# Kernel optimization log

Measured on AMD Instinct MI355X. Metric: run time of the kernel, lower is better.

Reference implementation:

```python
import jax, jax.numpy as jnp
import numpy as np

N_NODES = 50000   # gates in the circuit batch
N_HOPS = 100000   # number of k-hop cones
MAX_PI = 8        # max PIs per hop (padded, masked via stats == -1)
D = 128           # token_emb / hidden
D_FF = 4 * D      # cls_head hidden width (512)
TT = 64           # max_tt_len -> logits width
LN_EPS = 1e-5


def setup_inputs() -> dict:
    key = jax.random.key(0)
    ks = jax.random.split(key, 8)
    hf = jax.random.normal(ks[0], (N_NODES, D), jnp.float32)
    all_hop_pi = jax.random.randint(ks[1], (N_HOPS, MAX_PI), 0, N_NODES)
    # stats in {-1, 0, 1}; -1 marks an invalid (padded) PI slot
    all_hop_pi_stats = jax.random.randint(ks[2], (N_HOPS, MAX_PI), 0, 3) - 1
    all_hop_po = jax.random.randint(ks[3], (N_HOPS,), 0, N_NODES)
    w_q = jax.random.normal(ks[4], (D,), jnp.float32) / np.sqrt(D)
    W1 = jax.random.normal(ks[5], (D, D_FF), jnp.float32) / np.sqrt(D)
    b1 = jnp.zeros((D_FF,), jnp.float32)
    gamma = jnp.ones((D_FF,), jnp.float32)
    beta = jnp.zeros((D_FF,), jnp.float32)
    W2 = jax.random.normal(ks[6], (D_FF, TT), jnp.float32) / np.sqrt(D_FF)
    b2 = jnp.zeros((TT,), jnp.float32)
    return {
        'hf': hf, 'w_q': w_q, 'W1': W1, 'b1': b1, 'gamma': gamma,
        'beta': beta, 'W2': W2, 'b2': b2,
        'all_hop_pi': all_hop_pi, 'all_hop_pi_stats': all_hop_pi_stats,
        'all_hop_po': all_hop_po,
    }


def reference(hf, w_q, W1, b1, gamma, beta, W2, b2,
              all_hop_pi, all_hop_pi_stats, all_hop_po):
    # Per-hop gather: valid PI embeddings + PO embedding -> [H, P+1, D]
    pi_tok = hf[all_hop_pi]                       # [H, P, D]
    po_tok = hf[all_hop_po][:, None, :]           # [H, 1, D]
    tokens = jnp.concatenate([pi_tok, po_tok], axis=1)
    valid = jnp.concatenate(
        [all_hop_pi_stats != -1,
         jnp.ones((all_hop_po.shape[0], 1), bool)], axis=1)  # [H, P+1]
    # tf_Pooling: masked single-query attention pooling over the ragged set
    scores = jnp.einsum('hpd,d->hp', tokens, w_q) / jnp.sqrt(jnp.float32(D))
    scores = jnp.where(valid, scores, jnp.float32(-1e30))
    attn = jax.nn.softmax(scores, axis=-1)
    hop_hf = jnp.einsum('hp,hpd->hd', attn, tokens)  # [H, D]
    # cls_head: Linear(D, 4D) -> ReLU -> LayerNorm(4D) -> Linear(4D, TT)
    h = jax.nn.relu(hop_hf @ W1 + b1)
    mu = jnp.mean(h, axis=-1, keepdims=True)
    var = jnp.var(h, axis=-1, keepdims=True)
    h = (h - mu) * jax.lax.rsqrt(var + LN_EPS) * gamma + beta
    logits = h @ W2 + b2                           # [H, TT]
    return logits
```

## Files before the change

### kernel.cpp

```cpp
#include <hip/hip_runtime.h>
#include <hip/hip_bf16.h>
#include <math.h>

#define DIM 128
#define DFF 512
#define TTW 64
#define NPI 8
#define NTOK 9
#define POOL_HOPS 8
#define HEAD_HOPS 32

typedef __attribute__((ext_vector_type(8))) short short8;
typedef __attribute__((ext_vector_type(4))) float float4v;

__device__ __forceinline__ unsigned short f32_bf16(float f) {
    union { float f; unsigned u; } v; v.f = f;
    unsigned r = v.u + 0x7FFFu + ((v.u >> 16) & 1u);
    return (unsigned short)(r >> 16);
}
__device__ __forceinline__ float bf16lo_f32(unsigned u) {
    union { unsigned u; float f; } v; v.u = u << 16;
    return v.f;
}
__device__ __forceinline__ float bf16hi_f32(unsigned u) {
    union { unsigned u; float f; } v; v.u = u & 0xffff0000u;
    return v.f;
}
__device__ __forceinline__ unsigned pk_bf16(float a, float b) {
    __hip_bfloat162 h = __float22bfloat162_rn(float2{a, b});
    union { __hip_bfloat162 h; unsigned u; } cv; cv.h = h;
    return cv.u;
}

__global__ __launch_bounds__(256)
void prep_k(const float* __restrict__ hf, const float* __restrict__ W1,
            const float* __restrict__ W2, const int* __restrict__ pi,
            const int* __restrict__ stats,
            unsigned short* __restrict__ hf2, unsigned short* __restrict__ w1t,
            unsigned short* __restrict__ w2t, int* __restrict__ cpack,
            int n_hf, int B_HF, int n_pk)
{
    __shared__ float tile[32][33];
    const int b = blockIdx.x, t = threadIdx.x;
    if (b < B_HF) {
        int i = (b * 256 + t) * 4;
        if (i < n_hf) {
            float4v v = *(const float4v*)(hf + i);
            uint2 o;
            o.x = pk_bf16(v[0], v[1]);
            o.y = pk_bf16(v[2], v[3]);
            *(uint2*)(hf2 + i) = o;
        }
    } else if (b < B_HF + 64) {
        const int tb = b - B_HF;
        const int r0 = (tb & 3) * 32, c0 = (tb >> 2) * 32;
        const int ty = t >> 3, tx = t & 7;
        *(float4v*)&tile[ty][tx * 4] = *(const float4v*)(W1 + (r0 + ty) * DFF + c0 + tx * 4);
        __syncthreads();
        uint2 o;
        o.x = pk_bf16(tile[tx * 4 + 0][ty], tile[tx * 4 + 1][ty]);
        o.y = pk_bf16(tile[tx * 4 + 2][ty], tile[tx * 4 + 3][ty]);
        *(uint2*)(w1t + (c0 + ty) * DIM + r0 + tx * 4) = o;
    } else if (b < B_HF + 96) {
        const int tb = b - B_HF - 64;
        const int r0 = (tb & 15) * 32, c0 = (tb >> 4) * 32;
        const int ty = t >> 3, tx = t & 7;
        *(float4v*)&tile[ty][tx * 4] = *(const float4v*)(W2 + (r0 + ty) * TTW + c0 + tx * 4);
        __syncthreads();
        uint2 o;
        o.x = pk_bf16(tile[tx * 4 + 0][ty], tile[tx * 4 + 1][ty]);
        o.y = pk_bf16(tile[tx * 4 + 2][ty], tile[tx * 4 + 3][ty]);
        *(uint2*)(w2t + (c0 + ty) * DFF + r0 + tx * 4) = o;
    } else {
        const int pb = b - (B_HF + 96);
        int i = (pb * 256 + t) * 4;
        if (i < n_pk) {
            int4 p = *(const int4*)(pi + i);
            int4 s = *(const int4*)(stats + i);
            int4 o;
            o.x = p.x | (s.x == -1 ? (int)0x80000000 : 0);
            o.y = p.y | (s.y == -1 ? (int)0x80000000 : 0);
            o.z = p.z | (s.z == -1 ? (int)0x80000000 : 0);
            o.w = p.w | (s.w == -1 ? (int)0x80000000 : 0);
            *(int4*)(cpack + i) = o;
        }
    }
}

__global__ __launch_bounds__(256, 6)
void pool_k(const unsigned short* __restrict__ hf2,
            const float* __restrict__ w_q,
            const int* __restrict__ cpack,
            const int* __restrict__ po,
            unsigned short* __restrict__ pooled,
            int H)
{
    const int t = threadIdx.x;
    const int g = t >> 5, l = t & 31;
    const int hop = blockIdx.x * POOL_HOPS + g;
    if (hop >= H) return;

    const float4v wq4 = *(const float4v*)(w_q + l * 4);

    int idx[NTOK]; bool val[NTOK];
    {
        int4 c0 = *(const int4*)(cpack + hop * NPI);
        int4 c1 = *(const int4*)(cpack + hop * NPI + 4);
        idx[0]=c0.x & 0x7fffffff; val[0]=c0.x >= 0;
        idx[1]=c0.y & 0x7fffffff; val[1]=c0.y >= 0;
        idx[2]=c0.z & 0x7fffffff; val[2]=c0.z >= 0;
        idx[3]=c0.w & 0x7fffffff; val[3]=c0.w >= 0;
        idx[4]=c1.x & 0x7fffffff; val[4]=c1.x >= 0;
        idx[5]=c1.y & 0x7fffffff; val[5]=c1.y >= 0;
        idx[6]=c1.z & 0x7fffffff; val[6]=c1.z >= 0;
        idx[7]=c1.w & 0x7fffffff; val[7]=c1.w >= 0;
        idx[8]=po[hop]; val[8]=true;
    }
    uint2 tu[NTOK];
    #pragma unroll
    for (int p = 0; p < NTOK; ++p)
        tu[p] = *(const uint2*)(hf2 + (size_t)idx[p] * DIM + l * 4);

    float tok[NTOK][4];
    #pragma unroll
    for (int p = 0; p < NTOK; ++p) {
        tok[p][0] = bf16lo_f32(tu[p].x);
        tok[p][1] = bf16hi_f32(tu[p].x);
        tok[p][2] = bf16lo_f32(tu[p].y);
        tok[p][3] = bf16hi_f32(tu[p].y);
    }
    float sc[NTOK];
    #pragma unroll
    for (int p = 0; p < NTOK; ++p)
        sc[p] = tok[p][0]*wq4[0] + tok[p][1]*wq4[1]
              + tok[p][2]*wq4[2] + tok[p][3]*wq4[3];
    #pragma unroll
    for (int m = 1; m < 32; m <<= 1) {
        #pragma unroll
        for (int p = 0; p < NTOK; ++p) sc[p] += __shfl_xor(sc[p], m);
    }
    const float isd = 0.08838834764831845f;
    float mx = -1e30f;
    #pragma unroll
    for (int p = 0; p < NTOK; ++p) {
        sc[p] = val[p] ? sc[p] * isd : -1e30f;
        mx = fmaxf(mx, sc[p]);
    }
    float se = 0.f;
    #pragma unroll
    for (int p = 0; p < NTOK; ++p) { sc[p] = __expf(sc[p] - mx); se += sc[p]; }
    const float inv = 1.f / se;
    float a0=0.f, a1=0.f, a2=0.f, a3=0.f;
    #pragma unroll
    for (int p = 0; p < NTOK; ++p) {
        float a = sc[p] * inv;
        a0 += a * tok[p][0]; a1 += a * tok[p][1];
        a2 += a * tok[p][2]; a3 += a * tok[p][3];
    }
    uint2 o;
    o.x = pk_bf16(a0, a1);
    o.y = pk_bf16(a2, a3);
    *(uint2*)(pooled + (size_t)hop * DIM + l * 4) = o;
}

__global__ __launch_bounds__(256, 3)
void head_k(const unsigned short* __restrict__ pooled,
            const unsigned short* __restrict__ w1t,
            const float* __restrict__ b1,
            const float* __restrict__ gamma,
            const float* __restrict__ beta,
            const unsigned short* __restrict__ w2t,
            const float* __restrict__ b2,
            float* __restrict__ out,
            int H)
{
    __shared__ unsigned short Hsm[HEAD_HOPS][DFF + 8];
    __shared__ float part[2][16][4][2];

    const int t    = threadIdx.x;
    const int lane = t & 63;
    const int w    = t >> 6;
    const int row  = lane & 15;
    const int quad = lane >> 4;
    const int hop0 = blockIdx.x * HEAD_HOPS;

    float4v acc[8][2];
    #pragma unroll
    for (int mt = 0; mt < 8; ++mt) {
        acc[mt][0] = (float4v){0.f, 0.f, 0.f, 0.f};
        acc[mt][1] = (float4v){0.f, 0.f, 0.f, 0.f};
    }
    {
        short8 bfr[2][4];
        #pragma unroll
        for (int ks = 0; ks < 4; ++ks) {
            const int k0 = ks * 32 + quad * 8;
            #pragma unroll
            for (int ht = 0; ht < 2; ++ht) {
                int hp = hop0 + ht * 16 + row;
                if (hp >= H) hp = H - 1;
                bfr[ht][ks] = *(const short8*)(pooled + (size_t)hp * DIM + k0);
            }
        }
        #pragma unroll
        for (int mt = 0; mt < 8; ++mt) {
            const unsigned short* wrow = w1t + (size_t)(w * 128 + mt * 16 + row) * DIM;
            #pragma unroll
            for (int ks = 0; ks < 4; ++ks) {
                short8 afr = *(const short8*)(wrow + ks * 32 + quad * 8);
                acc[mt][0] = __builtin_amdgcn_mfma_f32_16x16x32_bf16(afr, bfr[0][ks], acc[mt][0], 0, 0, 0);
                acc[mt][1] = __builtin_amdgcn_mfma_f32_16x16x32_bf16(afr, bfr[1][ks], acc[mt][1], 0, 0, 0);
            }
        }
    }
    float sum0 = 0.f, ssq0 = 0.f, sum1 = 0.f, ssq1 = 0.f;
    #pragma unroll
    for (int mt = 0; mt < 8; ++mt) {
        const int nb = w * 128 + mt * 16 + quad * 4;
        const float4v bias = *(const float4v*)(b1 + nb);
        #pragma unroll
        for (int r = 0; r < 4; ++r) {
            float v0 = fmaxf(acc[mt][0][r] + bias[r], 0.f);
            float v1 = fmaxf(acc[mt][1][r] + bias[r], 0.f);
            acc[mt][0][r] = v0;  sum0 += v0;  ssq0 += v0 * v0;
            acc[mt][1][r] = v1;  sum1 += v1;  ssq1 += v1 * v1;
        }
    }
    #pragma unroll
    for (int m = 16; m <= 32; m <<= 1) {
        sum0 += __shfl_xor(sum0, m);  ssq0 += __shfl_xor(ssq0, m);
        sum1 += __shfl_xor(sum1, m);  ssq1 += __shfl_xor(ssq1, m);
    }
    if (lane < 16) {
        part[0][row][w][0] = sum0;  part[0][row][w][1] = ssq0;
        part[1][row][w][0] = sum1;  part[1][row][w][1] = ssq1;
    }
    __syncthreads();
    float mu[2], rs[2];
    #pragma unroll
    for (int ht = 0; ht < 2; ++ht) {
        float S = 0.f, Q = 0.f;
        #pragma unroll
        for (int ww = 0; ww < 4; ++ww) {
            S += part[ht][row][ww][0];
            Q += part[ht][row][ww][1];
        }
        const float invn = 1.f / (float)DFF;
        mu[ht] = S * invn;
        float var = Q * invn - mu[ht] * mu[ht];
        rs[ht] = rsqrtf(var + 1e-5f);
    }
    #pragma unroll
    for (int mt = 0; mt < 8; ++mt) {
        const int nb = w * 128 + mt * 16 + quad * 4;
        const float4v g4  = *(const float4v*)(gamma + nb);
        const float4v be4 = *(const float4v*)(beta + nb);
        #pragma unroll
        for (int ht = 0; ht < 2; ++ht) {
            float o[4];
            #pragma unroll
            for (int r = 0; r < 4; ++r) {
                float tg = rs[ht] * g4[r];
                o[r] = acc[mt][ht][r] * tg + (be4[r] - mu[ht] * tg);
            }
            uint2 p;
            p.x = pk_bf16(o[0], o[1]);
            p.y = pk_bf16(o[2], o[3]);
            *(uint2*)&Hsm[ht * 16 + row][nb] = p;
        }
    }
    __syncthreads();

    {
        float4v acc2[2];
        acc2[0] = (float4v){0.f,0.f,0.f,0.f};
        acc2[1] = (float4v){0.f,0.f,0.f,0.f};
        #pragma unroll
        for (int ks = 0; ks < 16; ++ks) {
            const int k0 = ks * 32 + quad * 8;
            short8 bfr = *(const short8*)(w2t + (size_t)(w * 16 + row) * DFF + k0);
            #pragma unroll
            for (int mt = 0; mt < 2; ++mt) {
                short8 afr = *(const short8*)&Hsm[mt * 16 + row][k0];
                acc2[mt] = __builtin_amdgcn_mfma_f32_16x16x32_bf16(
                    afr, bfr, acc2[mt], 0, 0, 0);
            }
        }
        const float bb = b2[w * 16 + row];
        #pragma unroll
        for (int mt = 0; mt < 2; ++mt) {
            #pragma unroll
            for (int r = 0; r < 4; ++r) {
                int hop = hop0 + mt * 16 + quad * 4 + r;
                if (hop < H)
                    out[(size_t)hop * TTW + w * 16 + row] = acc2[mt][r] + bb;
            }
        }
    }
}

extern "C" void kernel_launch(void* const* d_in, const int* in_sizes, int n_in,
                              void* d_out, int out_size, void* d_ws, size_t ws_size,
                              hipStream_t stream) {
    const float* hf    = (const float*)d_in[0];
    const float* w_q   = (const float*)d_in[1];
    const float* W1    = (const float*)d_in[2];
    const float* b1    = (const float*)d_in[3];
    const float* gamma = (const float*)d_in[4];
    const float* beta  = (const float*)d_in[5];
    const float* W2    = (const float*)d_in[6];
    const float* b2    = (const float*)d_in[7];
    const int* pi      = (const int*)d_in[8];
    const int* stats   = (const int*)d_in[9];
    const int* po      = (const int*)d_in[10];
    float* out         = (float*)d_out;

    const int n_hf = in_sizes[0];
    const int H    = in_sizes[10];
    const int n_pk = H * NPI;
    const int Hpad = ((H + HEAD_HOPS - 1) / HEAD_HOPS) * HEAD_HOPS;

    char* ws = (char*)d_ws;
    unsigned short* w1t    = (unsigned short*)ws;
    unsigned short* w2t    = (unsigned short*)(ws + 131072);
    unsigned short* hf2    = (unsigned short*)(ws + 196608);
    size_t off_cp = 196608 + ((size_t)n_hf * 2 + 255) / 256 * 256;
    int*            cpack  = (int*)(ws + off_cp);
    size_t off_pl = off_cp + ((size_t)n_pk * 4 + 255) / 256 * 256;
    unsigned short* pooled = (unsigned short*)(ws + off_pl);

    const int B_HF = (n_hf + 1023) / 1024;
    const int B_PK = (n_pk + 1023) / 1024;
    const int prep_blocks = B_HF + 96 + B_PK;

    hipLaunchKernelGGL(prep_k, dim3(prep_blocks), dim3(256), 0, stream,
                       hf, W1, W2, pi, stats, hf2, w1t, w2t, cpack,
                       n_hf, B_HF, n_pk);
    hipLaunchKernelGGL(pool_k, dim3((H + POOL_HOPS - 1) / POOL_HOPS), dim3(256), 0, stream,
                       hf2, w_q, cpack, po, pooled, H);
    hipLaunchKernelGGL(head_k, dim3(Hpad / HEAD_HOPS), dim3(256), 0, stream,
                       pooled, w1t, b1, gamma, beta, w2t, b2, out, H);
}
```

Baseline: 225.7 us.

## Fuse attention pooling into head kernel via shared-memory pooled tile

Merges the pooling and cls-head kernels into one. Each block pools its 32 hops into an LDS tile, then runs the MFMA head on that tile directly. This drops the global round-trip of the pooled bf16 buffer and one kernel launch. In exchange, gather latency now sits inside a kernel limited to occupancy 3 with extra LDS, so the pooling phase gets less latency hiding.

```diff
diff --git a/kernel.cpp b/kernel.cpp
--- a/kernel.cpp
+++ b/kernel.cpp
@@ -7,17 +7,11 @@
 #define TTW 64
 #define NPI 8
 #define NTOK 9
-#define POOL_HOPS 8
-#define HEAD_HOPS 32
+#define TILE_H 32
 
 typedef __attribute__((ext_vector_type(8))) short short8;
 typedef __attribute__((ext_vector_type(4))) float float4v;
 
-__device__ __forceinline__ unsigned short f32_bf16(float f) {
-    union { float f; unsigned u; } v; v.f = f;
-    unsigned r = v.u + 0x7FFFu + ((v.u >> 16) & 1u);
-    return (unsigned short)(r >> 16);
-}
 __device__ __forceinline__ float bf16lo_f32(unsigned u) {
     union { unsigned u; float f; } v; v.u = u << 16;
     return v.f;
@@ -87,94 +81,22 @@
     }
 }
 
-__global__ __launch_bounds__(256, 6)
-void pool_k(const unsigned short* __restrict__ hf2,
-            const float* __restrict__ w_q,
-            const int* __restrict__ cpack,
-            const int* __restrict__ po,
-            unsigned short* __restrict__ pooled,
-            int H)
+__global__ __launch_bounds__(256, 3)
+void fused_k(const unsigned short* __restrict__ hf2,
+             const float* __restrict__ w_q,
+             const int* __restrict__ cpack,
+             const int* __restrict__ po,
+             const unsigned short* __restrict__ w1t,
+             const float* __restrict__ b1,
+             const float* __restrict__ gamma,
+             const float* __restrict__ beta,
+             const unsigned short* __restrict__ w2t,
+             const float* __restrict__ b2,
+             float* __restrict__ out,
+             int H)
 {
-    const int t = threadIdx.x;
-    const int g = t >> 5, l = t & 31;
-    const int hop = blockIdx.x * POOL_HOPS + g;
-    if (hop >= H) return;
-
-    const float4v wq4 = *(const float4v*)(w_q + l * 4);
-
-    int idx[NTOK]; bool val[NTOK];
-    {
-        int4 c0 = *(const int4*)(cpack + hop * NPI);
-        int4 c1 = *(const int4*)(cpack + hop * NPI + 4);
-        idx[0]=c0.x & 0x7fffffff; val[0]=c0.x >= 0;
-        idx[1]=c0.y & 0x7fffffff; val[1]=c0.y >= 0;
-        idx[2]=c0.z & 0x7fffffff; val[2]=c0.z >= 0;
-        idx[3]=c0.w & 0x7fffffff; val[3]=c0.w >= 0;
-        idx[4]=c1.x & 0x7fffffff; val[4]=c1.x >= 0;
-        idx[5]=c1.y & 0x7fffffff; val[5]=c1.y >= 0;
-        idx[6]=c1.z & 0x7fffffff; val[6]=c1.z >= 0;
-        idx[7]=c1.w & 0x7fffffff; val[7]=c1.w >= 0;
-        idx[8]=po[hop]; val[8]=true;
-    }
-    uint2 tu[NTOK];
-    #pragma unroll
-    for (int p = 0; p < NTOK; ++p)
-        tu[p] = *(const uint2*)(hf2 + (size_t)idx[p] * DIM + l * 4);
-
-    float tok[NTOK][4];
-    #pragma unroll
-    for (int p = 0; p < NTOK; ++p) {
-        tok[p][0] = bf16lo_f32(tu[p].x);
-        tok[p][1] = bf16hi_f32(tu[p].x);
-        tok[p][2] = bf16lo_f32(tu[p].y);
-        tok[p][3] = bf16hi_f32(tu[p].y);
-    }
-    float sc[NTOK];
-    #pragma unroll
-    for (int p = 0; p < NTOK; ++p)
-        sc[p] = tok[p][0]*wq4[0] + tok[p][1]*wq4[1]
-              + tok[p][2]*wq4[2] + tok[p][3]*wq4[3];
-    #pragma unroll
-    for (int m = 1; m < 32; m <<= 1) {
-        #pragma unroll
-        for (int p = 0; p < NTOK; ++p) sc[p] += __shfl_xor(sc[p], m);
-    }
-    const float isd = 0.08838834764831845f;
-    float mx = -1e30f;
-    #pragma unroll
-    for (int p = 0; p < NTOK; ++p) {
-        sc[p] = val[p] ? sc[p] * isd : -1e30f;
-        mx = fmaxf(mx, sc[p]);
-    }
-    float se = 0.f;
-    #pragma unroll
-    for (int p = 0; p < NTOK; ++p) { sc[p] = __expf(sc[p] - mx); se += sc[p]; }
-    const float inv = 1.f / se;
-    float a0=0.f, a1=0.f, a2=0.f, a3=0.f;
-    #pragma unroll
-    for (int p = 0; p < NTOK; ++p) {
-        float a = sc[p] * inv;
-        a0 += a * tok[p][0]; a1 += a * tok[p][1];
-        a2 += a * tok[p][2]; a3 += a * tok[p][3];
-    }
-    uint2 o;
-    o.x = pk_bf16(a0, a1);
-    o.y = pk_bf16(a2, a3);
-    *(uint2*)(pooled + (size_t)hop * DIM + l * 4) = o;
-}
-
-__global__ __launch_bounds__(256, 3)
-void head_k(const unsigned short* __restrict__ pooled,
-            const unsigned short* __restrict__ w1t,
-            const float* __restrict__ b1,
-            const float* __restrict__ gamma,
-            const float* __restrict__ beta,
-            const unsigned short* __restrict__ w2t,
-            const float* __restrict__ b2,
-            float* __restrict__ out,
-            int H)
-{
-    __shared__ unsigned short Hsm[HEAD_HOPS][DFF + 8];
+    __shared__ unsigned short Apool[TILE_H][DIM + 8];
+    __shared__ unsigned short Hsm[TILE_H][DFF + 8];
     __shared__ float part[2][16][4][2];
 
     const int t    = threadIdx.x;
@@ -182,7 +104,76 @@
     const int w    = t >> 6;
     const int row  = lane & 15;
     const int quad = lane >> 4;
-    const int hop0 = blockIdx.x * HEAD_HOPS;
+    const int hop0 = blockIdx.x * TILE_H;
+
+    {
+        const int g = t >> 5, l = t & 31;
+        const float4v wq4 = *(const float4v*)(w_q + l * 4);
+        #pragma unroll
+        for (int it = 0; it < 4; ++it) {
+            const int hl = g + it * 8;
+            const int hop = hop0 + hl;
+            uint2 o = {0u, 0u};
+            if (hop < H) {
+                int idx[NTOK]; bool val[NTOK];
+                int4 c0 = *(const int4*)(cpack + hop * NPI);
+                int4 c1 = *(const int4*)(cpack + hop * NPI + 4);
+                idx[0]=c0.x & 0x7fffffff; val[0]=c0.x >= 0;
+                idx[1]=c0.y & 0x7fffffff; val[1]=c0.y >= 0;
+                idx[2]=c0.z & 0x7fffffff; val[2]=c0.z >= 0;
+                idx[3]=c0.w & 0x7fffffff; val[3]=c0.w >= 0;
+                idx[4]=c1.x & 0x7fffffff; val[4]=c1.x >= 0;
+                idx[5]=c1.y & 0x7fffffff; val[5]=c1.y >= 0;
+                idx[6]=c1.z & 0x7fffffff; val[6]=c1.z >= 0;
+                idx[7]=c1.w & 0x7fffffff; val[7]=c1.w >= 0;
+                idx[8]=po[hop]; val[8]=true;
+                uint2 tu[NTOK];
+                #pragma unroll
+                for (int p = 0; p < NTOK; ++p)
+                    tu[p] = *(const uint2*)(hf2 + (size_t)idx[p] * DIM + l * 4);
+                float tok[NTOK][4];
+                #pragma unroll
+                for (int p = 0; p < NTOK; ++p) {
+                    tok[p][0] = bf16lo_f32(tu[p].x);
+                    tok[p][1] = bf16hi_f32(tu[p].x);
+                    tok[p][2] = bf16lo_f32(tu[p].y);
+                    tok[p][3] = bf16hi_f32(tu[p].y);
+                }
+                float sc[NTOK];
+                #pragma unroll
+                for (int p = 0; p < NTOK; ++p)
+                    sc[p] = tok[p][0]*wq4[0] + tok[p][1]*wq4[1]
+                          + tok[p][2]*wq4[2] + tok[p][3]*wq4[3];
+                #pragma unroll
+                for (int m = 1; m < 32; m <<= 1) {
+                    #pragma unroll
+                    for (int p = 0; p < NTOK; ++p) sc[p] += __shfl_xor(sc[p], m);
+                }
+                const float isd = 0.08838834764831845f;
+                float mx = -1e30f;
+                #pragma unroll
+                for (int p = 0; p < NTOK; ++p) {
+                    sc[p] = val[p] ? sc[p] * isd : -1e30f;
+                    mx = fmaxf(mx, sc[p]);
+                }
+                float se = 0.f;
+                #pragma unroll
+                for (int p = 0; p < NTOK; ++p) { sc[p] = __expf(sc[p] - mx); se += sc[p]; }
+                const float inv = 1.f / se;
+                float a0=0.f, a1=0.f, a2=0.f, a3=0.f;
+                #pragma unroll
+                for (int p = 0; p < NTOK; ++p) {
+                    float a = sc[p] * inv;
+                    a0 += a * tok[p][0]; a1 += a * tok[p][1];
+                    a2 += a * tok[p][2]; a3 += a * tok[p][3];
+                }
+                o.x = pk_bf16(a0, a1);
+                o.y = pk_bf16(a2, a3);
+            }
+            *(uint2*)&Apool[hl][l * 4] = o;
+        }
+    }
+    __syncthreads();
 
     float4v acc[8][2];
     #pragma unroll
@@ -196,11 +187,8 @@
         for (int ks = 0; ks < 4; ++ks) {
             const int k0 = ks * 32 + quad * 8;
             #pragma unroll
-            for (int ht = 0; ht < 2; ++ht) {
-                int hp = hop0 + ht * 16 + row;
-                if (hp >= H) hp = H - 1;
-                bfr[ht][ks] = *(const short8*)(pooled + (size_t)hp * DIM + k0);
-            }
+            for (int ht = 0; ht < 2; ++ht)
+                bfr[ht][ks] = *(const short8*)&Apool[ht * 16 + row][k0];
         }
         #pragma unroll
         for (int mt = 0; mt < 8; ++mt) {
@@ -318,7 +306,6 @@
     const int n_hf = in_sizes[0];
     const int H    = in_sizes[10];
     const int n_pk = H * NPI;
-    const int Hpad = ((H + HEAD_HOPS - 1) / HEAD_HOPS) * HEAD_HOPS;
 
     char* ws = (char*)d_ws;
     unsigned short* w1t    = (unsigned short*)ws;
@@ -326,8 +313,6 @@
     unsigned short* hf2    = (unsigned short*)(ws + 196608);
     size_t off_cp = 196608 + ((size_t)n_hf * 2 + 255) / 256 * 256;
     int*            cpack  = (int*)(ws + off_cp);
-    size_t off_pl = off_cp + ((size_t)n_pk * 4 + 255) / 256 * 256;
-    unsigned short* pooled = (unsigned short*)(ws + off_pl);
 
     const int B_HF = (n_hf + 1023) / 1024;
     const int B_PK = (n_pk + 1023) / 1024;
@@ -336,8 +321,6 @@
     hipLaunchKernelGGL(prep_k, dim3(prep_blocks), dim3(256), 0, stream,
                        hf, W1, W2, pi, stats, hf2, w1t, w2t, cpack,
                        n_hf, B_HF, n_pk);
-    hipLaunchKernelGGL(pool_k, dim3((H + POOL_HOPS - 1) / POOL_HOPS), dim3(256), 0, stream,
-                       hf2, w_q, cpack, po, pooled, H);
-    hipLaunchKernelGGL(head_k, dim3(Hpad / HEAD_HOPS), dim3(256), 0, stream,
-                       pooled, w1t, b1, gamma, beta, w2t, b2, out, H);
-}
+    hipLaunchKernelGGL(fused_k, dim3((H + TILE_H - 1) / TILE_H), dim3(256), 0, stream,
+                       hf2, w_q, cpack, po, w1t, b1, gamma, beta, w2t, b2, out, H);
+}
```

Result: faster. 212.4 us (-5.9%).
